# Kernel tuning notes

Hardware: AMD Instinct MI355X
Metric: run time of the kernel (lower is better)

## Reference

```python
import jax, jax.numpy as jnp
import numpy as np

N_HEADS = 8
D_TIME = 128
D_TGT = 128
D_KEYS = D_TIME // N_HEADS  # 16
LN_EPS = 1e-5


def _layer_norm(x, gamma, beta):
    mu = jnp.mean(x, axis=-1, keepdims=True)
    var = jnp.var(x, axis=-1, keepdims=True)
    return (x - mu) * jax.lax.rsqrt(var + LN_EPS) * gamma + beta


def setup_inputs() -> dict:
    key = jax.random.key(0)
    ks = jax.random.split(key, 16)
    B, N, L, D = 4, 207, 64, D_TIME
    s = 1.0 / np.sqrt(D)
    inp = {
        "time_features_Q": jax.random.normal(ks[0], (B, N, L, D), jnp.float32),
        "time_features_K": jax.random.normal(ks[1], (B, N, L, D), jnp.float32),
        "target_features_K": jax.random.normal(ks[2], (B, N, L, D_TGT), jnp.float32),
        # Linear weights stored as [in, out] (y = x @ W + b)
        "Wq": jax.random.normal(ks[3], (D, D), jnp.float32) * s,
        "bq": jnp.zeros((D,), jnp.float32),
        "Wk": jax.random.normal(ks[4], (D, D), jnp.float32) * s,
        "bk": jnp.zeros((D,), jnp.float32),
        "Wv": jax.random.normal(ks[5], (D, D), jnp.float32) * s,
        "bv": jnp.zeros((D,), jnp.float32),
        "Wot": jax.random.normal(ks[6], (D, D), jnp.float32) * s,
        "bot": jnp.zeros((D,), jnp.float32),
        "Wtg": jax.random.normal(ks[7], (D_TGT, D_TGT), jnp.float32) * s,
        "btg": jnp.zeros((D_TGT,), jnp.float32),
        "g_time": jnp.ones((D,), jnp.float32),
        "b_time": jnp.zeros((D,), jnp.float32),
        "g_tgt": jnp.ones((D_TGT,), jnp.float32),
        "b_tgt": jnp.zeros((D_TGT,), jnp.float32),
    }
    return inp


def reference(time_features_Q, time_features_K, target_features_K,
              Wq, bq, Wk, bk, Wv, bv, Wot, bot, Wtg, btg,
              g_time, b_time, g_tgt, b_tgt):
    B, N, Lq, D = time_features_Q.shape
    Lk = time_features_K.shape[2]
    H, dk = N_HEADS, D_KEYS

    def split_heads(x, d):
        # [B,N,L,H*d] -> [B,N,H,L,d]
        return x.reshape(B, N, -1, H, d).transpose(0, 1, 3, 2, 4)

    q = split_heads(time_features_Q @ Wq + bq, dk)
    k = split_heads(time_features_K @ Wk + bk, dk)
    v = split_heads(time_features_K @ Wv + bv, dk)

    # Unnormalized scores (no softmax), scaled by sqrt(d_keys)
    attn_score = jnp.einsum('bnhqd,bnhkd->bnhqk', q, k) / np.sqrt(dk)

    # Time branch: score @ values -> merge heads -> proj -> (dropout=eval noop) -> residual + LN
    tv = jnp.einsum('bnhqk,bnhkd->bnhqd', attn_score, v)
    tv = tv.transpose(0, 1, 3, 2, 4).reshape(B, N, Lq, D)
    tv = tv @ Wot + bot
    time_value = _layer_norm(tv + time_features_Q, g_time, b_time)

    # Target branch: reuse the same score tensor on raw target features
    Dt = target_features_K.shape[-1]
    tk = target_features_K.reshape(B, N, Lk, H, Dt // H).transpose(0, 1, 3, 2, 4)
    ct = jnp.einsum('bnhqk,bnhkd->bnhqd', attn_score, tk)
    ct = ct.transpose(0, 1, 3, 2, 4).reshape(B, N, Lq, Dt)
    ct = ct @ Wtg + btg
    cross_target = _layer_norm(ct, g_tgt, b_tgt)

    return attn_score, time_value, cross_target
```

## Files before the change

kernel.cpp:

```cpp
#include <hip/hip_runtime.h>

typedef float f32x4 __attribute__((ext_vector_type(4)));
typedef short s16x4 __attribute__((ext_vector_type(4)));
typedef short s16x8 __attribute__((ext_vector_type(8)));

#define SA 136
#define ST 72

__device__ __forceinline__ short f2bf(float f) {
    union { float f; unsigned u; } c; c.f = f;
    return (short)((c.u + 0x7FFFu + ((c.u >> 16) & 1u)) >> 16);
}

__global__ __launch_bounds__(256) void k_prep(
    const float* __restrict__ Wq, const float* __restrict__ Wk,
    const float* __restrict__ Wv, const float* __restrict__ Wot,
    const float* __restrict__ Wtg, short* __restrict__ Wt) {
    const float* srcs[5] = {Wq, Wk, Wv, Wot, Wtg};
    const float* W = srcs[blockIdx.x];
    short* dst = Wt + blockIdx.x * 16384;
    const int t = threadIdx.x;
#pragma unroll 4
    for (int i = 0; i < 64; ++i) {
        int idx = i * 256 + t;
        int k = idx >> 7, n = idx & 127;
        dst[n * 128 + k] = f2bf(W[idx]);
    }
}

__device__ __forceinline__ s16x8 wfrag(const short* __restrict__ Wt,
                                       int ni, int kk, int m, int quad) {
    return *(const s16x8*)(Wt + (ni * 16 + m) * 128 + kk * 32 + quad * 8);
}

__global__ __launch_bounds__(256) void k_main(
    const float* __restrict__ XQ, const float* __restrict__ XK,
    const float* __restrict__ Tgt, const short* __restrict__ Wt,
    const float* __restrict__ bq, const float* __restrict__ bk,
    const float* __restrict__ bv, const float* __restrict__ bot,
    const float* __restrict__ btg,
    const float* __restrict__ g_time, const float* __restrict__ b_time,
    const float* __restrict__ g_tgt, const float* __restrict__ b_tgt,
    float* __restrict__ out0, float* __restrict__ out1, float* __restrict__ out2) {
    const int bn = blockIdx.x;
    const int t = threadIdx.x;
    const int w = t >> 6, lane = t & 63, m = lane & 15, quad = lane >> 4;

    __shared__ short R1[64 * SA];
    __shared__ short R2[64 * SA];
    __shared__ short R3[128 * ST];
    __shared__ short R4[64 * ST];
    __shared__ short R5[16 * ST];

    const size_t base = (size_t)bn * 8192;
    const short* Wqt = Wt;
    const short* Wkt = Wt + 16384;
    const short* Wvt = Wt + 32768;
    const short* Wot_t = Wt + 49152;
    const short* Wtg_t = Wt + 65536;

    {
        const float* src = XK + base;
#pragma unroll
        for (int it = 0; it < 8; ++it) {
            int e = t + it * 256;
            f32x4 x = *(const f32x4*)(src + e * 4);
            int row = e >> 5, col = (e & 31) * 4;
            s16x4 p; p[0] = f2bf(x[0]); p[1] = f2bf(x[1]);
            p[2] = f2bf(x[2]); p[3] = f2bf(x[3]);
            *(s16x4*)(R3 + row * SA + col) = p;
        }
    }
    __syncthreads();

    {
        s16x8 a[4];
#pragma unroll
        for (int kk = 0; kk < 4; ++kk)
            a[kk] = *(const s16x8*)(R3 + (w * 16 + m) * SA + kk * 32 + quad * 8);

        f32x4 acck[8], accv[8];
#pragma unroll
        for (int ni = 0; ni < 8; ++ni) {
            acck[ni] = (f32x4){0.f, 0.f, 0.f, 0.f};
            accv[ni] = (f32x4){0.f, 0.f, 0.f, 0.f};
#pragma unroll
            for (int kk = 0; kk < 4; ++kk) {
                acck[ni] = __builtin_amdgcn_mfma_f32_16x16x32_bf16(
                    a[kk], wfrag(Wkt, ni, kk, m, quad), acck[ni], 0, 0, 0);
                accv[ni] = __builtin_amdgcn_mfma_f32_16x16x32_bf16(
                    a[kk], wfrag(Wvt, ni, kk, m, quad), accv[ni], 0, 0, 0);
            }
        }
#pragma unroll
        for (int ni = 0; ni < 8; ++ni) {
            const float bb = bk[ni * 16 + m];
#pragma unroll
            for (int r = 0; r < 4; ++r)
                R2[(w * 16 + quad * 4 + r) * SA + ni * 16 + m] = f2bf(acck[ni][r] + bb);
        }
        __syncthreads();
#pragma unroll
        for (int ni = 0; ni < 8; ++ni) {
            const float bb = bv[ni * 16 + m];
#pragma unroll
            for (int r = 0; r < 4; ++r)
                R3[(ni * 16 + m) * ST + w * 16 + quad * 4 + r] = f2bf(accv[ni][r] + bb);
        }
    }

    {
        const float* src = XQ + base;
#pragma unroll
        for (int it = 0; it < 8; ++it) {
            int e = t + it * 256;
            f32x4 x = *(const f32x4*)(src + e * 4);
            int row = e >> 5, col = (e & 31) * 4;
            s16x4 p; p[0] = f2bf(x[0]); p[1] = f2bf(x[1]);
            p[2] = f2bf(x[2]); p[3] = f2bf(x[3]);
            *(s16x4*)(R1 + row * SA + col) = p;
        }
    }
    __syncthreads();
    {
        s16x8 a[4];
#pragma unroll
        for (int kk = 0; kk < 4; ++kk)
            a[kk] = *(const s16x8*)(R1 + (w * 16 + m) * SA + kk * 32 + quad * 8);
        f32x4 accq[8];
#pragma unroll
        for (int ni = 0; ni < 8; ++ni) {
            accq[ni] = (f32x4){0.f, 0.f, 0.f, 0.f};
#pragma unroll
            for (int kk = 0; kk < 4; ++kk)
                accq[ni] = __builtin_amdgcn_mfma_f32_16x16x32_bf16(
                    a[kk], wfrag(Wqt, ni, kk, m, quad), accq[ni], 0, 0, 0);
        }
        __syncthreads();
#pragma unroll
        for (int ni = 0; ni < 8; ++ni) {
            const float bb = bq[ni * 16 + m];
#pragma unroll
            for (int r = 0; r < 4; ++r)
                R1[(w * 16 + quad * 4 + r) * SA + ni * 16 + m] = f2bf(accq[ni][r] + bb);
        }
    }
    __syncthreads();

    f32x4 accv8[8], acct8[8];
    const s16x8 zfrag = (s16x8){0, 0, 0, 0, 0, 0, 0, 0};
#pragma unroll
    for (int h = 0; h < 8; ++h) {
        {
            int key = t >> 2, c0 = (t & 3) * 4;
            f32x4 x = *(const f32x4*)(Tgt + base + key * 128 + h * 16 + c0);
#pragma unroll
            for (int r = 0; r < 4; ++r) R5[(c0 + r) * ST + key] = f2bf(x[r]);
        }
        __syncthreads();

        s16x8 aq = zfrag;
        if (quad < 2)
            aq = *(const s16x8*)(R1 + (w * 16 + m) * SA + h * 16 + quad * 8);
#pragma unroll
        for (int nj = 0; nj < 4; ++nj) {
            s16x8 bk_ = zfrag;
            if (quad < 2)
                bk_ = *(const s16x8*)(R2 + (nj * 16 + m) * SA + h * 16 + quad * 8);
            f32x4 s = __builtin_amdgcn_mfma_f32_16x16x32_bf16(
                aq, bk_, (f32x4){0.f, 0.f, 0.f, 0.f}, 0, 0, 0);
#pragma unroll
            for (int r = 0; r < 4; ++r) {
                const int row = w * 16 + quad * 4 + r;
                const float sval = s[r] * 0.25f;
                out0[(size_t)bn * 32768 + h * 4096 + row * 64 + nj * 16 + m] = sval;
                R4[row * ST + nj * 16 + m] = f2bf(sval);
            }
        }

        accv8[h] = (f32x4){0.f, 0.f, 0.f, 0.f};
        acct8[h] = (f32x4){0.f, 0.f, 0.f, 0.f};
#pragma unroll
        for (int kk = 0; kk < 2; ++kk) {
            s16x8 a  = *(const s16x8*)(R4 + (w * 16 + m) * ST + kk * 32 + quad * 8);
            s16x8 bv_ = *(const s16x8*)(R3 + (h * 16 + m) * ST + kk * 32 + quad * 8);
            s16x8 bt_ = *(const s16x8*)(R5 + m * ST + kk * 32 + quad * 8);
            accv8[h] = __builtin_amdgcn_mfma_f32_16x16x32_bf16(a, bv_, accv8[h], 0, 0, 0);
            acct8[h] = __builtin_amdgcn_mfma_f32_16x16x32_bf16(a, bt_, acct8[h], 0, 0, 0);
        }
        __syncthreads();
    }

#pragma unroll
    for (int h = 0; h < 8; ++h) {
#pragma unroll
        for (int r = 0; r < 4; ++r) {
            const int row = w * 16 + quad * 4 + r;
            R1[row * SA + h * 16 + m] = f2bf(accv8[h][r]);
            R2[row * SA + h * 16 + m] = f2bf(acct8[h][r]);
        }
    }
    __syncthreads();

#pragma unroll
    for (int br = 0; br < 2; ++br) {
        const short* sA = br == 0 ? R1 : R2;
        const short* Wp = br == 0 ? Wot_t : Wtg_t;
        const float* bias = br == 0 ? bot : btg;
        const float* gam = br == 0 ? g_time : g_tgt;
        const float* bet = br == 0 ? b_time : b_tgt;
        float* outp = (br == 0 ? out1 : out2) + base;
        const float* resid = br == 0 ? XQ + base : nullptr;

        s16x8 a[4];
#pragma unroll
        for (int kk = 0; kk < 4; ++kk)
            a[kk] = *(const s16x8*)(sA + (w * 16 + m) * SA + kk * 32 + quad * 8);
        f32x4 acc[8];
#pragma unroll
        for (int ni = 0; ni < 8; ++ni) {
            acc[ni] = (f32x4){0.f, 0.f, 0.f, 0.f};
#pragma unroll
            for (int kk = 0; kk < 4; ++kk)
                acc[ni] = __builtin_amdgcn_mfma_f32_16x16x32_bf16(
                    a[kk], wfrag(Wp, ni, kk, m, quad), acc[ni], 0, 0, 0);
        }
        float y[8][4];
        float s1[4] = {0.f, 0.f, 0.f, 0.f}, s2[4] = {0.f, 0.f, 0.f, 0.f};
#pragma unroll
        for (int ni = 0; ni < 8; ++ni) {
            const int col = ni * 16 + m;
            const float bb = bias[col];
#pragma unroll
            for (int r = 0; r < 4; ++r) {
                const int row = w * 16 + quad * 4 + r;
                float v = acc[ni][r] + bb;
                if (resid) v += resid[row * 128 + col];
                y[ni][r] = v;
                s1[r] += v;
                s2[r] += v * v;
            }
        }
#pragma unroll
        for (int mask = 1; mask < 16; mask <<= 1) {
#pragma unroll
            for (int r = 0; r < 4; ++r) {
                s1[r] += __shfl_xor(s1[r], mask, 64);
                s2[r] += __shfl_xor(s2[r], mask, 64);
            }
        }
        float mu[4], rstd[4];
#pragma unroll
        for (int r = 0; r < 4; ++r) {
            mu[r] = s1[r] * (1.0f / 128.0f);
            float var = s2[r] * (1.0f / 128.0f) - mu[r] * mu[r];
            rstd[r] = rsqrtf(var + 1e-5f);
        }
#pragma unroll
        for (int ni = 0; ni < 8; ++ni) {
            const int col = ni * 16 + m;
            const float g = gam[col], bb = bet[col];
#pragma unroll
            for (int r = 0; r < 4; ++r) {
                const int row = w * 16 + quad * 4 + r;
                outp[row * 128 + col] = (y[ni][r] - mu[r]) * rstd[r] * g + bb;
            }
        }
    }
}

extern "C" void kernel_launch(void* const* d_in, const int* in_sizes, int n_in,
                              void* d_out, int out_size, void* d_ws, size_t ws_size,
                              hipStream_t stream) {
    const float* XQ  = (const float*)d_in[0];
    const float* XK  = (const float*)d_in[1];
    const float* Tgt = (const float*)d_in[2];
    const float* Wq  = (const float*)d_in[3];
    const float* bq  = (const float*)d_in[4];
    const float* Wk  = (const float*)d_in[5];
    const float* bk  = (const float*)d_in[6];
    const float* Wv  = (const float*)d_in[7];
    const float* bv  = (const float*)d_in[8];
    const float* Wot = (const float*)d_in[9];
    const float* bot = (const float*)d_in[10];
    const float* Wtg = (const float*)d_in[11];
    const float* btg = (const float*)d_in[12];
    const float* g_time = (const float*)d_in[13];
    const float* b_time = (const float*)d_in[14];
    const float* g_tgt  = (const float*)d_in[15];
    const float* b_tgt  = (const float*)d_in[16];

    const int BN = in_sizes[0] / 8192;

    short* Wt = (short*)d_ws;

    float* out0 = (float*)d_out;
    float* out1 = out0 + (size_t)BN * 32768;
    float* out2 = out1 + (size_t)BN * 8192;

    k_prep<<<5, 256, 0, stream>>>(Wq, Wk, Wv, Wot, Wtg, Wt);
    k_main<<<BN, 256, 0, stream>>>(XQ, XK, Tgt, Wt, bq, bk, bv, bot, btg,
                                   g_time, b_time, g_tgt, b_tgt,
                                   out0, out1, out2);
}
```

Baseline: 349.0 us.

## Load MFMA operands straight from global, swizzle LDS, use per-wave score buffers

```diff
diff --git a/kernel.cpp b/kernel.cpp
--- a/kernel.cpp
+++ b/kernel.cpp
@@ -4,12 +4,16 @@
 typedef short s16x4 __attribute__((ext_vector_type(4)));
 typedef short s16x8 __attribute__((ext_vector_type(8)));
 
-#define SA 136
-#define ST 72
-
 __device__ __forceinline__ short f2bf(float f) {
     union { float f; unsigned u; } c; c.f = f;
     return (short)((c.u + 0x7FFFu + ((c.u >> 16) & 1u)) >> 16);
+}
+
+__device__ __forceinline__ int swz128(int row, int col) {
+    return row * 128 + (col ^ ((row & 7) << 3));
+}
+__device__ __forceinline__ int swz64(int row, int col) {
+    return row * 64 + (col ^ ((row & 7) << 3));
 }
 
 __global__ __launch_bounds__(256) void k_prep(
@@ -33,7 +37,16 @@
     return *(const s16x8*)(Wt + (ni * 16 + m) * 128 + kk * 32 + quad * 8);
 }
 
-__global__ __launch_bounds__(256) void k_main(
+__device__ __forceinline__ s16x8 ldfrag(const float* __restrict__ src, int row, int col) {
+    f32x4 x0 = *(const f32x4*)(src + row * 128 + col);
+    f32x4 x1 = *(const f32x4*)(src + row * 128 + col + 4);
+    s16x8 p;
+    p[0] = f2bf(x0[0]); p[1] = f2bf(x0[1]); p[2] = f2bf(x0[2]); p[3] = f2bf(x0[3]);
+    p[4] = f2bf(x1[0]); p[5] = f2bf(x1[1]); p[6] = f2bf(x1[2]); p[7] = f2bf(x1[3]);
+    return p;
+}
+
+__global__ __launch_bounds__(256, 3) void k_main(
     const float* __restrict__ XQ, const float* __restrict__ XK,
     const float* __restrict__ Tgt, const short* __restrict__ Wt,
     const float* __restrict__ bq, const float* __restrict__ bk,
@@ -45,12 +58,12 @@
     const int bn = blockIdx.x;
     const int t = threadIdx.x;
     const int w = t >> 6, lane = t & 63, m = lane & 15, quad = lane >> 4;
-
-    __shared__ short R1[64 * SA];
-    __shared__ short R2[64 * SA];
-    __shared__ short R3[128 * ST];
-    __shared__ short R4[64 * ST];
-    __shared__ short R5[16 * ST];
+    const int r0 = w * 16;
+
+    __shared__ short Rk[64 * 128];
+    __shared__ short Rv[128 * 64];
+    __shared__ short Rs[4][16 * 64];
+    __shared__ short Rt[4][16 * 64];
 
     const size_t base = (size_t)bn * 8192;
     const short* Wqt = Wt;
@@ -58,27 +71,44 @@
     const short* Wvt = Wt + 32768;
     const short* Wot_t = Wt + 49152;
     const short* Wtg_t = Wt + 65536;
-
-    {
-        const float* src = XK + base;
-#pragma unroll
-        for (int it = 0; it < 8; ++it) {
-            int e = t + it * 256;
-            f32x4 x = *(const f32x4*)(src + e * 4);
-            int row = e >> 5, col = (e & 31) * 4;
-            s16x4 p; p[0] = f2bf(x[0]); p[1] = f2bf(x[1]);
-            p[2] = f2bf(x[2]); p[3] = f2bf(x[3]);
-            *(s16x4*)(R3 + row * SA + col) = p;
-        }
-    }
-    __syncthreads();
-
+    short* myRs = Rs[w];
+    short* myRt = Rt[w];
+
+    s16x8 qf[8];
     {
         s16x8 a[4];
 #pragma unroll
         for (int kk = 0; kk < 4; ++kk)
-            a[kk] = *(const s16x8*)(R3 + (w * 16 + m) * SA + kk * 32 + quad * 8);
-
+            a[kk] = ldfrag(XQ + base, r0 + m, kk * 32 + quad * 8);
+        f32x4 accq[8];
+#pragma unroll
+        for (int ni = 0; ni < 8; ++ni) {
+            accq[ni] = (f32x4){0.f, 0.f, 0.f, 0.f};
+#pragma unroll
+            for (int kk = 0; kk < 4; ++kk)
+                accq[ni] = __builtin_amdgcn_mfma_f32_16x16x32_bf16(
+                    a[kk], wfrag(Wqt, ni, kk, m, quad), accq[ni], 0, 0, 0);
+        }
+#pragma unroll
+        for (int ni = 0; ni < 8; ++ni) {
+            const float bb = bq[ni * 16 + m];
+#pragma unroll
+            for (int r = 0; r < 4; ++r)
+                Rk[swz128(r0 + quad * 4 + r, ni * 16 + m)] = f2bf(accq[ni][r] + bb);
+        }
+#pragma unroll
+        for (int h = 0; h < 8; ++h) {
+            qf[h] = (s16x8){0, 0, 0, 0, 0, 0, 0, 0};
+            if (quad < 2)
+                qf[h] = *(const s16x8*)(Rk + swz128(r0 + m, h * 16 + quad * 8));
+        }
+    }
+
+    {
+        s16x8 a[4];
+#pragma unroll
+        for (int kk = 0; kk < 4; ++kk)
+            a[kk] = ldfrag(XK + base, r0 + m, kk * 32 + quad * 8);
         f32x4 acck[8], accv[8];
 #pragma unroll
         for (int ni = 0; ni < 8; ++ni) {
@@ -94,87 +124,47 @@
         }
 #pragma unroll
         for (int ni = 0; ni < 8; ++ni) {
-            const float bb = bk[ni * 16 + m];
-#pragma unroll
-            for (int r = 0; r < 4; ++r)
-                R2[(w * 16 + quad * 4 + r) * SA + ni * 16 + m] = f2bf(acck[ni][r] + bb);
-        }
-        __syncthreads();
-#pragma unroll
-        for (int ni = 0; ni < 8; ++ni) {
-            const float bb = bv[ni * 16 + m];
-#pragma unroll
-            for (int r = 0; r < 4; ++r)
-                R3[(ni * 16 + m) * ST + w * 16 + quad * 4 + r] = f2bf(accv[ni][r] + bb);
-        }
-    }
-
-    {
-        const float* src = XQ + base;
-#pragma unroll
-        for (int it = 0; it < 8; ++it) {
-            int e = t + it * 256;
-            f32x4 x = *(const f32x4*)(src + e * 4);
-            int row = e >> 5, col = (e & 31) * 4;
-            s16x4 p; p[0] = f2bf(x[0]); p[1] = f2bf(x[1]);
-            p[2] = f2bf(x[2]); p[3] = f2bf(x[3]);
-            *(s16x4*)(R1 + row * SA + col) = p;
-        }
-    }
-    __syncthreads();
-    {
-        s16x8 a[4];
-#pragma unroll
-        for (int kk = 0; kk < 4; ++kk)
-            a[kk] = *(const s16x8*)(R1 + (w * 16 + m) * SA + kk * 32 + quad * 8);
-        f32x4 accq[8];
-#pragma unroll
-        for (int ni = 0; ni < 8; ++ni) {
-            accq[ni] = (f32x4){0.f, 0.f, 0.f, 0.f};
-#pragma unroll
-            for (int kk = 0; kk < 4; ++kk)
-                accq[ni] = __builtin_amdgcn_mfma_f32_16x16x32_bf16(
-                    a[kk], wfrag(Wqt, ni, kk, m, quad), accq[ni], 0, 0, 0);
-        }
-        __syncthreads();
-#pragma unroll
-        for (int ni = 0; ni < 8; ++ni) {
-            const float bb = bq[ni * 16 + m];
-#pragma unroll
-            for (int r = 0; r < 4; ++r)
-                R1[(w * 16 + quad * 4 + r) * SA + ni * 16 + m] = f2bf(accq[ni][r] + bb);
+            const float bbk = bk[ni * 16 + m];
+            const float bbv = bv[ni * 16 + m];
+#pragma unroll
+            for (int r = 0; r < 4; ++r) {
+                Rk[swz128(r0 + quad * 4 + r, ni * 16 + m)] = f2bf(acck[ni][r] + bbk);
+                Rv[swz64(ni * 16 + m, r0 + quad * 4 + r)] = f2bf(accv[ni][r] + bbv);
+            }
         }
     }
     __syncthreads();
 
     f32x4 accv8[8], acct8[8];
     const s16x8 zfrag = (s16x8){0, 0, 0, 0, 0, 0, 0, 0};
+    float* o0 = out0 + (size_t)bn * 32768;
 #pragma unroll
     for (int h = 0; h < 8; ++h) {
         {
-            int key = t >> 2, c0 = (t & 3) * 4;
-            f32x4 x = *(const f32x4*)(Tgt + base + key * 128 + h * 16 + c0);
-#pragma unroll
-            for (int r = 0; r < 4; ++r) R5[(c0 + r) * ST + key] = f2bf(x[r]);
-        }
-        __syncthreads();
-
-        s16x8 aq = zfrag;
-        if (quad < 2)
-            aq = *(const s16x8*)(R1 + (w * 16 + m) * SA + h * 16 + quad * 8);
+            const int c0 = (lane & 3) * 4;
+#pragma unroll
+            for (int it = 0; it < 4; ++it) {
+                const int key = (lane >> 2) + it * 16;
+                f32x4 x = *(const f32x4*)(Tgt + base + key * 128 + h * 16 + c0);
+#pragma unroll
+                for (int r = 0; r < 4; ++r) myRt[swz64(c0 + r, key)] = f2bf(x[r]);
+            }
+        }
+
+        const s16x8 aq = qf[h];
 #pragma unroll
         for (int nj = 0; nj < 4; ++nj) {
             s16x8 bk_ = zfrag;
             if (quad < 2)
-                bk_ = *(const s16x8*)(R2 + (nj * 16 + m) * SA + h * 16 + quad * 8);
+                bk_ = *(const s16x8*)(Rk + swz128(nj * 16 + m, h * 16 + quad * 8));
             f32x4 s = __builtin_amdgcn_mfma_f32_16x16x32_bf16(
                 aq, bk_, (f32x4){0.f, 0.f, 0.f, 0.f}, 0, 0, 0);
 #pragma unroll
             for (int r = 0; r < 4; ++r) {
-                const int row = w * 16 + quad * 4 + r;
+                const int row = r0 + quad * 4 + r;
                 const float sval = s[r] * 0.25f;
-                out0[(size_t)bn * 32768 + h * 4096 + row * 64 + nj * 16 + m] = sval;
-                R4[row * ST + nj * 16 + m] = f2bf(sval);
+                o0[h * 4096 + row * 64 + nj * 16 + m] = sval;
+                myRs[swz64(quad * 4 + r, nj * 16 + m)] = f2bf(sval);
             }
         }
 
@@ -182,29 +172,29 @@
         acct8[h] = (f32x4){0.f, 0.f, 0.f, 0.f};
 #pragma unroll
         for (int kk = 0; kk < 2; ++kk) {
-            s16x8 a  = *(const s16x8*)(R4 + (w * 16 + m) * ST + kk * 32 + quad * 8);
-            s16x8 bv_ = *(const s16x8*)(R3 + (h * 16 + m) * ST + kk * 32 + quad * 8);
-            s16x8 bt_ = *(const s16x8*)(R5 + m * ST + kk * 32 + quad * 8);
-            accv8[h] = __builtin_amdgcn_mfma_f32_16x16x32_bf16(a, bv_, accv8[h], 0, 0, 0);
-            acct8[h] = __builtin_amdgcn_mfma_f32_16x16x32_bf16(a, bt_, acct8[h], 0, 0, 0);
-        }
-        __syncthreads();
-    }
-
+            s16x8 sa  = *(const s16x8*)(myRs + swz64(m, kk * 32 + quad * 8));
+            s16x8 bv_ = *(const s16x8*)(Rv + swz64(h * 16 + m, kk * 32 + quad * 8));
+            s16x8 bt_ = *(const s16x8*)(myRt + swz64(m, kk * 32 + quad * 8));
+            accv8[h] = __builtin_amdgcn_mfma_f32_16x16x32_bf16(sa, bv_, accv8[h], 0, 0, 0);
+            acct8[h] = __builtin_amdgcn_mfma_f32_16x16x32_bf16(sa, bt_, acct8[h], 0, 0, 0);
+        }
+    }
+    __syncthreads();
+
+    short* Rct = Rv;
 #pragma unroll
     for (int h = 0; h < 8; ++h) {
 #pragma unroll
         for (int r = 0; r < 4; ++r) {
-            const int row = w * 16 + quad * 4 + r;
-            R1[row * SA + h * 16 + m] = f2bf(accv8[h][r]);
-            R2[row * SA + h * 16 + m] = f2bf(acct8[h][r]);
-        }
-    }
-    __syncthreads();
+            const int row = r0 + quad * 4 + r;
+            Rk[swz128(row, h * 16 + m)]  = f2bf(accv8[h][r]);
+            Rct[swz128(row, h * 16 + m)] = f2bf(acct8[h][r]);
+        }
+    }
 
 #pragma unroll
     for (int br = 0; br < 2; ++br) {
-        const short* sA = br == 0 ? R1 : R2;
+        const short* sA = br == 0 ? Rk : Rct;
         const short* Wp = br == 0 ? Wot_t : Wtg_t;
         const float* bias = br == 0 ? bot : btg;
         const float* gam = br == 0 ? g_time : g_tgt;
@@ -215,7 +205,7 @@
         s16x8 a[4];
 #pragma unroll
         for (int kk = 0; kk < 4; ++kk)
-            a[kk] = *(const s16x8*)(sA + (w * 16 + m) * SA + kk * 32 + quad * 8);
+            a[kk] = *(const s16x8*)(sA + swz128(r0 + m, kk * 32 + quad * 8));
         f32x4 acc[8];
 #pragma unroll
         for (int ni = 0; ni < 8; ++ni) {
@@ -233,7 +223,7 @@
             const float bb = bias[col];
 #pragma unroll
             for (int r = 0; r < 4; ++r) {
-                const int row = w * 16 + quad * 4 + r;
+                const int row = r0 + quad * 4 + r;
                 float v = acc[ni][r] + bb;
                 if (resid) v += resid[row * 128 + col];
                 y[ni][r] = v;
@@ -262,7 +252,7 @@
             const float g = gam[col], bb = bet[col];
 #pragma unroll
             for (int r = 0; r < 4; ++r) {
-                const int row = w * 16 + quad * 4 + r;
+                const int row = r0 + quad * 4 + r;
                 outp[row * 128 + col] = (y[ni][r] - mu[r]) * rstd[r] * g + bb;
             }
         }
```

After: 436.8 us. 1.25x slower.
